# Performance work log

Measured on AMD Instinct MI355X. Metric: run time of the kernel, lower is better.

The kernel has to match this reference:

```python
import jax, jax.numpy as jnp
import numpy as np

N_HEAD = 16


def _rope_cos_sin(T, head_dim, dtype):
    inv_freq = 1.0 / (10000.0 ** (jnp.arange(0, head_dim, 2, dtype=jnp.float32) / head_dim))
    t = jnp.arange(T, dtype=jnp.float32)
    freqs = jnp.outer(t, inv_freq)  # [T, head_dim//2]
    return jnp.cos(freqs).astype(dtype), jnp.sin(freqs).astype(dtype)


def _apply_rope(x, cos, sin):
    # x: [B, H, T, D]; cos/sin: [T, D//2]
    x_even = x[..., ::2]
    x_odd = x[..., 1::2]
    c = cos[None, None, :, :]
    s = sin[None, None, :, :]
    out_even = x_even * c - x_odd * s
    out_odd = x_even * s + x_odd * c
    # interleave back: [..., D//2, 2] -> [..., D]
    return jnp.stack((out_even, out_odd), axis=-1).reshape(x.shape)


def setup_inputs() -> dict:
    key = jax.random.key(0)
    k1, k2, k3 = jax.random.split(key, 3)
    B, T, C = 2, 2048, 1024
    x = jax.random.normal(k1, (B, T, C), dtype=jnp.float32)
    w_qkv = jax.random.normal(k2, (C, 3 * C), dtype=jnp.float32) * (1.0 / np.sqrt(C))
    w_proj = jax.random.normal(k3, (C, C), dtype=jnp.float32) * (1.0 / np.sqrt(C))
    b_proj = jnp.zeros((C,), dtype=jnp.float32)
    return {"x": x, "w_qkv": w_qkv, "w_proj": w_proj, "b_proj": b_proj}


def reference(x, w_qkv, w_proj, b_proj):
    B, T, C = x.shape
    H = N_HEAD
    D = C // H
    qkv = x @ w_qkv  # [B, T, 3C]
    q, k, v = jnp.split(qkv, 3, axis=2)
    # [B, T, C] -> [B, H, T, D]
    q = q.reshape(B, T, H, D).transpose(0, 2, 1, 3)
    k = k.reshape(B, T, H, D).transpose(0, 2, 1, 3)
    v = v.reshape(B, T, H, D).transpose(0, 2, 1, 3)
    cos, sin = _rope_cos_sin(T, D, q.dtype)
    q = _apply_rope(q, cos, sin)
    k = _apply_rope(k, cos, sin)
    # causal SDPA
    scale = 1.0 / np.sqrt(D)
    att = jnp.einsum('bhqd,bhkd->bhqk', q, k) * scale
    causal = jnp.tril(jnp.ones((T, T), dtype=bool))
    att = jnp.where(causal[None, None, :, :], att, jnp.finfo(att.dtype).min)
    att = jax.nn.softmax(att, axis=-1)
    y = jnp.einsum('bhqk,bhkd->bhqd', att, v)  # [B, H, T, D]
    y = y.transpose(0, 2, 1, 3).reshape(B, T, C)
    return y @ w_proj + b_proj
```

## Files before the change

kernel.cpp:

```cpp
#include <hip/hip_runtime.h>
#include <math.h>

#define T_SEQ 2048
#define CDIM  1024
#define HEADS 16
#define DHEAD 64
#define BATCH 2
#define M_ROWS 4096
#define QSCALE 0.18033688011112042f

typedef unsigned short u16;
typedef unsigned int u32;
typedef __attribute__((ext_vector_type(8))) short bf16x8;
typedef __attribute__((ext_vector_type(4))) float f32x4;
typedef __attribute__((ext_vector_type(16))) float f32x16;

__device__ inline u16 f2bf(float f) {
    u32 u = __builtin_bit_cast(u32, f);
    u32 r = (u + 0x7fffu + ((u >> 16) & 1u)) >> 16;
    return (u16)r;
}

__device__ inline u32 cvtpk(float lo, float hi) {
    u32 r;
    asm("v_cvt_pk_bf16_f32 %0, %1, %2" : "=v"(r) : "v"(lo), "v"(hi));
    return r;
}

__device__ inline void permswap(u32& x, u32& y) {
    asm volatile("v_permlane32_swap_b32 %0, %1" : "+v"(x), "+v"(y));
}

__device__ inline float fexp2(float x) {
#if __has_builtin(__builtin_amdgcn_exp2f)
    return __builtin_amdgcn_exp2f(x);
#else
    float r; asm("v_exp_f32 %0, %1" : "=v"(r) : "v"(x)); return r;
#endif
}

__device__ inline void gload16(const void* g, void* l) {
    __builtin_amdgcn_global_load_lds(
        (const __attribute__((address_space(1))) void*)g,
        (__attribute__((address_space(3))) void*)l, 16, 0, 0);
}

__global__ void rope_table_kernel(float* __restrict__ cosT, float* __restrict__ sinT) {
    int idx = blockIdx.x * blockDim.x + threadIdx.x;
    if (idx >= T_SEQ * 32) return;
    int t = idx >> 5;
    int i = idx & 31;
    float expo = (2.0f * (float)i) / 64.0f;
    float inv = powf(10000.0f, -expo);
    float a = (float)t * inv;
    cosT[idx] = cosf(a);
    sinT[idx] = sinf(a);
}

__global__ __launch_bounds__(256)
void conv_bf16(const float* __restrict__ in, u16* __restrict__ out, int n8) {
    int i = blockIdx.x * blockDim.x + threadIdx.x;
    if (i >= n8) return;
    const float4* p = (const float4*)(in + (size_t)i * 8);
    float4 a = p[0], b = p[1];
    uint4 o;
    o.x = (u32)f2bf(a.x) | ((u32)f2bf(a.y) << 16);
    o.y = (u32)f2bf(a.z) | ((u32)f2bf(a.w) << 16);
    o.z = (u32)f2bf(b.x) | ((u32)f2bf(b.y) << 16);
    o.w = (u32)f2bf(b.z) | ((u32)f2bf(b.w) << 16);
    *(uint4*)(out + (size_t)i * 8) = o;
}

__global__ __launch_bounds__(256)
void convT64(const float* __restrict__ in, u16* __restrict__ out, int K, int N) {
    __shared__ float Ls[64][65];
    const int tid = threadIdx.x;
    const int k0 = blockIdx.y << 6, n0 = blockIdx.x << 6;
    const int r0 = tid >> 4, c4 = (tid & 15) << 2;
#pragma unroll
    for (int p = 0; p < 4; p++) {
        int r = r0 + (p << 4);
        float4 v = *(const float4*)&in[(size_t)(k0 + r) * N + n0 + c4];
        Ls[r][c4 + 0] = v.x; Ls[r][c4 + 1] = v.y;
        Ls[r][c4 + 2] = v.z; Ls[r][c4 + 3] = v.w;
    }
    __syncthreads();
    const int n = tid >> 2, kq = (tid & 3) << 4;
    u32 pk[8];
#pragma unroll
    for (int j = 0; j < 8; j++) {
        float lo = Ls[kq + 2 * j][n], hi = Ls[kq + 2 * j + 1][n];
        pk[j] = (u32)f2bf(lo) | ((u32)f2bf(hi) << 16);
    }
    u32* dst = (u32*)&out[(size_t)(n0 + n) * K + k0 + kq];
    ((uint4*)dst)[0] = make_uint4(pk[0], pk[1], pk[2], pk[3]);
    ((uint4*)dst)[1] = make_uint4(pk[4], pk[5], pk[6], pk[7]);
}

__global__ __launch_bounds__(256)
void transposeV(const u16* __restrict__ in, u16* __restrict__ out) {
    __shared__ u16 Ls[64][72];
    const int tid = threadIdx.x;
    const int bh = blockIdx.y;
    const int t0 = blockIdx.x << 6;
    const u16* src = in + ((size_t)bh << 17) + ((size_t)t0 << 6);
#pragma unroll
    for (int p = 0; p < 2; p++) {
        int L = tid + (p << 8);
        int t = L >> 3, c = L & 7;
        uint4 v = *(const uint4*)&src[(size_t)t * 64 + (c << 3)];
        *(uint4*)&Ls[t][c << 3] = v;
    }
    __syncthreads();
    const int d = tid >> 2, tq = (tid & 3) << 4;
    u32 pk[8];
#pragma unroll
    for (int j = 0; j < 8; j++) {
        u16 lo = Ls[tq + 2 * j][d], hi = Ls[tq + 2 * j + 1][d];
        pk[j] = (u32)lo | ((u32)hi << 16);
    }
    u16* dst = out + ((size_t)bh << 17) + ((size_t)d << 11) + t0 + tq;
    ((uint4*)dst)[0] = make_uint4(pk[0], pk[1], pk[2], pk[3]);
    ((uint4*)dst)[1] = make_uint4(pk[4], pk[5], pk[6], pk[7]);
}

template <int EPI>
__global__ __launch_bounds__(256)
void gemm_bf16(const u16* __restrict__ A, const u16* __restrict__ Bt,
               int N, int K,
               const float* __restrict__ bias, float* __restrict__ outF,
               u16* __restrict__ qOut, u16* __restrict__ kOut, u16* __restrict__ vOut,
               const float* __restrict__ cosT, const float* __restrict__ sinT) {
    __shared__ u16 Alds[2][128 * 32];
    __shared__ u16 Blds[2][128 * 32];
    const int tid = threadIdx.x;
    const int lane = tid & 63;
    const int w = tid >> 6;
    const int wr = w >> 1, wc = w & 1;
    const int g = lane >> 4, l15 = lane & 15;
    const int m0 = blockIdx.y * 128, n0 = blockIdx.x * 128;

    f32x4 acc[4][4];
#pragma unroll
    for (int m = 0; m < 4; m++)
#pragma unroll
        for (int n = 0; n < 4; n++)
#pragma unroll
            for (int e = 0; e < 4; e++) acc[m][n][e] = 0.f;

    int aoff[4], boff[4];
#pragma unroll
    for (int m = 0; m < 4; m++) {
        aoff[m] = ((wr << 6) + (m << 4) + l15) * 64 + (g << 4);
        boff[m] = ((wc << 6) + (m << 4) + l15) * 64 + (g << 4);
    }
    const int rowA0 = tid >> 2, kk0 = (tid & 3) << 3;

#define GSTAGE(BUF, K0)                                                          \
    {                                                                            \
        _Pragma("unroll") for (int pq = 0; pq < 2; pq++) {                       \
            int L = tid + (pq << 8);                                             \
            int row = rowA0 + (pq << 6);                                         \
            gload16(A + (size_t)(m0 + row) * K + (K0) + kk0, &Alds[BUF][0] + L * 8); \
            gload16(Bt + (size_t)(n0 + row) * K + (K0) + kk0, &Blds[BUF][0] + L * 8); \
        }                                                                        \
    }

    GSTAGE(0, 0);
    const int nt = K >> 5;
    int cur = 0;
    for (int t = 0; t < nt; t++) {
        if (t + 1 < nt) {
            GSTAGE(cur ^ 1, ((t + 1) << 5));
            asm volatile("s_waitcnt vmcnt(4)" ::: "memory");
        } else {
            asm volatile("s_waitcnt vmcnt(0)" ::: "memory");
        }
        __builtin_amdgcn_s_barrier();
        asm volatile("" ::: "memory");
        bf16x8 af[4], bfr[4];
#pragma unroll
        for (int m = 0; m < 4; m++) af[m] = *(const bf16x8*)((const char*)&Alds[cur][0] + aoff[m]);
#pragma unroll
        for (int n = 0; n < 4; n++) bfr[n] = *(const bf16x8*)((const char*)&Blds[cur][0] + boff[n]);
#pragma unroll
        for (int m = 0; m < 4; m++)
#pragma unroll
            for (int n = 0; n < 4; n++)
                acc[m][n] = __builtin_amdgcn_mfma_f32_16x16x32_bf16(af[m], bfr[n], acc[m][n], 0, 0, 0);
        asm volatile("" ::: "memory");
        __builtin_amdgcn_s_barrier();
        cur ^= 1;
    }
#undef GSTAGE

    if (EPI == 0) {
        const int sec = n0 >> 10;
#pragma unroll
        for (int m = 0; m < 4; m++) {
#pragma unroll
            for (int j = 0; j < 4; j++) {
                int t = m0 + (wr << 6) + (m << 4) + (g << 2) + j;
                int b = t >> 11, tt = t & 2047;
#pragma unroll
                for (int n = 0; n < 4; n++) {
                    int cc = (n0 + (wc << 6) + (n << 4) + l15) & 1023;
                    int h = cc >> 6, d = cc & 63;
                    float val = acc[m][n][j];
                    float o = val;
                    if (sec < 2) {
                        float partner = __shfl_xor(val, 1);
                        int i0 = d >> 1;
                        float c = cosT[tt * 32 + i0], s = sinT[tt * 32 + i0];
                        o = ((d & 1) == 0) ? (val * c - partner * s)
                                           : (partner * s + val * c);
                        if (sec == 0) o *= QSCALE;
                    }
                    size_t off = (((size_t)((b * 16 + h) * 2048 + tt)) << 6) + d;
                    u16* dst = (sec == 0) ? qOut : ((sec == 1) ? kOut : vOut);
                    dst[off] = f2bf(o);
                }
            }
        }
    } else {
#pragma unroll
        for (int m = 0; m < 4; m++) {
#pragma unroll
            for (int j = 0; j < 4; j++) {
                int t = m0 + (wr << 6) + (m << 4) + (g << 2) + j;
#pragma unroll
                for (int n = 0; n < 4; n++) {
                    int col = n0 + (wc << 6) + (n << 4) + l15;
                    outF[(size_t)t * N + col] = acc[m][n][j] + bias[col];
                }
            }
        }
    }
}

__device__ __forceinline__ void kv_stage2(const u16* Kb, const u16* Vtb,
                                          u16* Kl, u16* Vl, int tid, int k0) {
#pragma unroll
    for (int pp = 0; pp < 4; pp++) {
        int L = tid + (pp << 7);
        int row = L >> 3, c = L & 7;
        int cg = (c ^ (row & 7)) << 3;
        gload16(Kb + (((size_t)(k0 + row)) << 6) + cg, Kl + L * 8);
        gload16(Vtb + ((size_t)row << 11) + k0 + cg, Vl + L * 8);
    }
}

template <int NS>
__device__ __forceinline__ void attn_step32(
    const bf16x8 (&qf)[4], f32x16 (&O)[2], float& MR, float& LR,
    const char* Kl, const char* Vl, const int (&foff)[2][4],
    int lim, bool diag) {
    f32x16 st[NS];
#pragma unroll
    for (int s = 0; s < NS; s++) {
#pragma unroll
        for (int e = 0; e < 16; e++) st[s][e] = 0.f;
#pragma unroll
        for (int ks = 0; ks < 4; ks++) {
            bf16x8 kf = *(const bf16x8*)(Kl + foff[s][ks]);
            st[s] = __builtin_amdgcn_mfma_f32_32x32x16_bf16(kf, qf[ks], st[s], 0, 0, 0);
        }
    }
    if (diag) {
#pragma unroll
        for (int r = 0; r < 16; r++) {
            const int kvloc = (r & 3) + 8 * (r >> 2);
            if (kvloc > lim) st[NS - 1][r] = -1e30f;
        }
    }
    float t8[8];
#pragma unroll
    for (int r = 0; r < 8; r++) {
        float a = fmaxf(st[0][r], st[0][r + 8]);
        if (NS == 2) a = fmaxf(a, fmaxf(st[1][r], st[1][r + 8]));
        t8[r] = a;
    }
    float m = fmaxf(fmaxf(fmaxf(t8[0], t8[4]), fmaxf(t8[1], t8[5])),
                    fmaxf(fmaxf(t8[2], t8[6]), fmaxf(t8[3], t8[7])));
    m = fmaxf(m, __shfl_xor(m, 32));
    float mn = fmaxf(MR, m);
    if (__ballot(m - MR > 10.f)) {
        float al = fexp2(MR - mn);
        MR = mn;
        LR *= al;
#pragma unroll
        for (int e = 0; e < 16; e++) { O[0][e] *= al; O[1][e] *= al; }
    }
    float s0 = 0.f, s1 = 0.f, s2 = 0.f, s3 = 0.f;
#pragma unroll
    for (int s = 0; s < NS; s++)
#pragma unroll
        for (int r = 0; r < 16; r++) {
            float pv = fexp2(st[s][r] - MR);
            st[s][r] = pv;
            if ((r & 3) == 0) s0 += pv;
            else if ((r & 3) == 1) s1 += pv;
            else if ((r & 3) == 2) s2 += pv;
            else s3 += pv;
        }
    float sum = (s0 + s1) + (s2 + s3);
    sum += __shfl_xor(sum, 32);
    LR += sum;
#pragma unroll
    for (int ks = 0; ks < 2 * NS; ks++) {
        const int sT = ks >> 1, b1 = (ks & 1) << 3;
        u32 a = cvtpk(st[sT][b1 + 0], st[sT][b1 + 1]);
        u32 b = cvtpk(st[sT][b1 + 2], st[sT][b1 + 3]);
        u32 c = cvtpk(st[sT][b1 + 4], st[sT][b1 + 5]);
        u32 d = cvtpk(st[sT][b1 + 6], st[sT][b1 + 7]);
        permswap(a, c);
        permswap(b, d);
        bf16x8 pf = __builtin_bit_cast(bf16x8, make_uint4(a, b, c, d));
#pragma unroll
        for (int t2 = 0; t2 < 2; t2++) {
            bf16x8 vf = *(const bf16x8*)(Vl + foff[t2][ks]);
            O[t2] = __builtin_amdgcn_mfma_f32_32x32x16_bf16(vf, pf, O[t2], 0, 0, 0);
        }
    }
}

__device__ __forceinline__ void attn_store32(
    const f32x16 (&O)[2], float LR, u16* __restrict__ Yg,
    int b, int hd, int q, int hl) {
    float inv = 1.0f / LR;
    size_t rowoff = (((size_t)(b * 2048 + q)) << 10) + (hd << 6);
#pragma unroll
    for (int t2 = 0; t2 < 2; t2++)
#pragma unroll
        for (int rg = 0; rg < 4; rg++) {
            int d0 = (rg << 3) + (hl << 2) + (t2 << 5);
            u32 lo = cvtpk(O[t2][4 * rg + 0] * inv, O[t2][4 * rg + 1] * inv);
            u32 hi = cvtpk(O[t2][4 * rg + 2] * inv, O[t2][4 * rg + 3] * inv);
            *(uint2*)&Yg[rowoff + d0] = make_uint2(lo, hi);
        }
}

__global__ __launch_bounds__(128)
void attn_mfma(const u16* __restrict__ Qg, const u16* __restrict__ Kg,
               const u16* __restrict__ Vtg, u16* __restrict__ Yg) {
    __shared__ u16 Ks[2][64 * 64];
    __shared__ u16 Vts[2][64 * 64];

    const int tid = threadIdx.x;
    const int lane = tid & 63;
    const int w = tid >> 6;
    const int l31 = lane & 31, hl = lane >> 5;
    const int p = blockIdx.x;
    const int bh = blockIdx.y;
    const int b = bh >> 4, hd = bh & 15;
    const int qtA = p, qtB = 31 - p;
    const int lim = l31 - (hl << 2);

    const u16* Qb = Qg + ((size_t)bh << 17);
    const u16* Kb = Kg + ((size_t)bh << 17);
    const u16* Vtb = Vtg + ((size_t)bh << 17);

    int foff[2][4];
#pragma unroll
    for (int s = 0; s < 2; s++)
#pragma unroll
        for (int ks = 0; ks < 4; ks++) {
            int row = (s << 5) + l31;
            foff[s][ks] = row * 128 + (((hl + (ks << 1)) ^ (row & 7)) << 4);
        }

    const int qrA = (qtA << 6) + (w << 5) + l31;
    const int qrB = (qtB << 6) + (w << 5) + l31;
    bf16x8 qfA[4], qfB[4];
#pragma unroll
    for (int ks = 0; ks < 4; ks++) {
        int co = (hl << 3) + (ks << 4);
        qfA[ks] = *(const bf16x8*)(Qb + (((size_t)qrA) << 6) + co);
        qfB[ks] = *(const bf16x8*)(Qb + (((size_t)qrB) << 6) + co);
    }

    kv_stage2(Kb, Vtb, &Ks[0][0], &Vts[0][0], tid, 0);
    int cur = 0;

    f32x16 O[2];
    float MR, LR;

#pragma unroll
    for (int e = 0; e < 16; e++) { O[0][e] = 0.f; O[1][e] = 0.f; }
    MR = -1e30f; LR = 0.f;
    for (int kt = 0; kt <= qtA; kt++) {
        int nk0 = (kt < qtA) ? ((kt + 1) << 6) : 0;
        kv_stage2(Kb, Vtb, &Ks[cur ^ 1][0], &Vts[cur ^ 1][0], tid, nk0);
        asm volatile("s_waitcnt vmcnt(8)" ::: "memory");
        __builtin_amdgcn_s_barrier();
        asm volatile("" ::: "memory");
        if (kt == qtA) {
            if (w == 0)
                attn_step32<1>(qfA, O, MR, LR, (const char*)&Ks[cur][0],
                               (const char*)&Vts[cur][0], foff, lim, true);
            else
                attn_step32<2>(qfA, O, MR, LR, (const char*)&Ks[cur][0],
                               (const char*)&Vts[cur][0], foff, lim, true);
        } else {
            attn_step32<2>(qfA, O, MR, LR, (const char*)&Ks[cur][0],
                           (const char*)&Vts[cur][0], foff, lim, false);
        }
        asm volatile("" ::: "memory");
        __builtin_amdgcn_s_barrier();
        cur ^= 1;
    }
    attn_store32(O, LR, Yg, b, hd, qrA, hl);

#pragma unroll
    for (int e = 0; e < 16; e++) { O[0][e] = 0.f; O[1][e] = 0.f; }
    MR = -1e30f; LR = 0.f;
    for (int kt = 0; kt <= qtB; kt++) {
        if (kt < qtB) {
            kv_stage2(Kb, Vtb, &Ks[cur ^ 1][0], &Vts[cur ^ 1][0], tid, (kt + 1) << 6);
            asm volatile("s_waitcnt vmcnt(8)" ::: "memory");
        } else {
            asm volatile("s_waitcnt vmcnt(0)" ::: "memory");
        }
        __builtin_amdgcn_s_barrier();
        asm volatile("" ::: "memory");
        if (kt == qtB) {
            if (w == 0)
                attn_step32<1>(qfB, O, MR, LR, (const char*)&Ks[cur][0],
                               (const char*)&Vts[cur][0], foff, lim, true);
            else
                attn_step32<2>(qfB, O, MR, LR, (const char*)&Ks[cur][0],
                               (const char*)&Vts[cur][0], foff, lim, true);
        } else {
            attn_step32<2>(qfB, O, MR, LR, (const char*)&Ks[cur][0],
                           (const char*)&Vts[cur][0], foff, lim, false);
        }
        asm volatile("" ::: "memory");
        __builtin_amdgcn_s_barrier();
        cur ^= 1;
    }
    attn_store32(O, LR, Yg, b, hd, qrB, hl);
}

extern "C" void kernel_launch(void* const* d_in, const int* in_sizes, int n_in,
                              void* d_out, int out_size, void* d_ws, size_t ws_size,
                              hipStream_t stream) {
    const float* x      = (const float*)d_in[0];
    const float* w_qkv  = (const float*)d_in[1];
    const float* w_proj = (const float*)d_in[2];
    const float* b_proj = (const float*)d_in[3];
    float* out = (float*)d_out;

    const size_t SZ = (size_t)M_ROWS * CDIM;
    char* ws = (char*)d_ws;
    u16* xb     = (u16*)ws;                ws += SZ * 2;
    u16* wqkvT  = (u16*)ws;                ws += (size_t)3 * CDIM * CDIM * 2;
    u16* wprojT = (u16*)ws;                ws += (size_t)CDIM * CDIM * 2;
    u16* Qb     = (u16*)ws;                ws += SZ * 2;
    u16* Kb     = (u16*)ws;                ws += SZ * 2;
    u16* Vb     = (u16*)ws;                ws += SZ * 2;
    u16* Vt     = (u16*)ws;                ws += SZ * 2;
    u16* Yb     = (u16*)ws;                ws += SZ * 2;
    float* cosT = (float*)ws;              ws += (size_t)T_SEQ * 32 * 4;
    float* sinT = (float*)ws;              ws += (size_t)T_SEQ * 32 * 4;

    rope_table_kernel<<<dim3(256), dim3(256), 0, stream>>>(cosT, sinT);
    conv_bf16<<<dim3(2048), dim3(256), 0, stream>>>(x, xb, (int)(SZ / 8));
    convT64<<<dim3(48, 16), dim3(256), 0, stream>>>(w_qkv, wqkvT, CDIM, 3 * CDIM);
    convT64<<<dim3(16, 16), dim3(256), 0, stream>>>(w_proj, wprojT, CDIM, CDIM);

    gemm_bf16<0><<<dim3(24, 32), dim3(256), 0, stream>>>(
        xb, wqkvT, 3 * CDIM, CDIM, nullptr, nullptr, Qb, Kb, Vb, cosT, sinT);

    transposeV<<<dim3(32, 32), dim3(256), 0, stream>>>(Vb, Vt);

    attn_mfma<<<dim3(16, 32), dim3(128), 0, stream>>>(Qb, Kb, Vt, Yb);

    gemm_bf16<1><<<dim3(8, 32), dim3(256), 0, stream>>>(
        Yb, wprojT, CDIM, CDIM, b_proj, out, nullptr, nullptr, nullptr, nullptr, nullptr);
}
```

Measured before the change: 230.2 us.

## Restructure causal attention into 128-row query blocks with 4 waves per block

Replaces the paired-tile attention scheme (2 waves, each block walking a short and a long query tile) with one 128-query block of 4 waves that share each staged K/V tile. Blocks are launched longest-first by reversing the query-block index, and waves skip or mask tiles according to their own 32-row slice. s_setprio hints are added around the MFMA sections. The aim is to halve K/V staging traffic per query and raise occupancy. The cost is more blocks with uneven work and some wave idling on diagonal tiles.

```diff
diff --git a/kernel.cpp b/kernel.cpp
--- a/kernel.cpp
+++ b/kernel.cpp
@@ -241,8 +241,8 @@
 __device__ __forceinline__ void kv_stage2(const u16* Kb, const u16* Vtb,
                                           u16* Kl, u16* Vl, int tid, int k0) {
 #pragma unroll
-    for (int pp = 0; pp < 4; pp++) {
-        int L = tid + (pp << 7);
+    for (int pp = 0; pp < 2; pp++) {
+        int L = tid + (pp << 8);
         int row = L >> 3, c = L & 7;
         int cg = (c ^ (row & 7)) << 3;
         gload16(Kb + (((size_t)(k0 + row)) << 6) + cg, Kl + L * 8);
@@ -250,14 +250,14 @@
     }
 }
 
-template <int NS>
+template <bool MASKED>
 __device__ __forceinline__ void attn_step32(
     const bf16x8 (&qf)[4], f32x16 (&O)[2], float& MR, float& LR,
-    const char* Kl, const char* Vl, const int (&foff)[2][4],
-    int lim, bool diag) {
-    f32x16 st[NS];
-#pragma unroll
-    for (int s = 0; s < NS; s++) {
+    const char* Kl, const char* Vl, const int (&foff)[2][4], int lim) {
+    f32x16 st[2];
+    __builtin_amdgcn_s_setprio(1);
+#pragma unroll
+    for (int s = 0; s < 2; s++) {
 #pragma unroll
         for (int e = 0; e < 16; e++) st[s][e] = 0.f;
 #pragma unroll
@@ -266,20 +266,23 @@
             st[s] = __builtin_amdgcn_mfma_f32_32x32x16_bf16(kf, qf[ks], st[s], 0, 0, 0);
         }
     }
-    if (diag) {
-#pragma unroll
-        for (int r = 0; r < 16; r++) {
-            const int kvloc = (r & 3) + 8 * (r >> 2);
-            if (kvloc > lim) st[NS - 1][r] = -1e30f;
+    __builtin_amdgcn_s_setprio(0);
+    if (MASKED) {
+#pragma unroll
+        for (int s = 0; s < 2; s++) {
+            const int ls = lim - (s << 5);
+#pragma unroll
+            for (int r = 0; r < 16; r++) {
+                const int kvloc = (r & 3) + 8 * (r >> 2);
+                if (kvloc > ls) st[s][r] = -1e30f;
+            }
         }
     }
     float t8[8];
 #pragma unroll
-    for (int r = 0; r < 8; r++) {
-        float a = fmaxf(st[0][r], st[0][r + 8]);
-        if (NS == 2) a = fmaxf(a, fmaxf(st[1][r], st[1][r + 8]));
-        t8[r] = a;
-    }
+    for (int r = 0; r < 8; r++)
+        t8[r] = fmaxf(fmaxf(st[0][r], st[0][r + 8]),
+                      fmaxf(st[1][r], st[1][r + 8]));
     float m = fmaxf(fmaxf(fmaxf(t8[0], t8[4]), fmaxf(t8[1], t8[5])),
                     fmaxf(fmaxf(t8[2], t8[6]), fmaxf(t8[3], t8[7])));
     m = fmaxf(m, __shfl_xor(m, 32));
@@ -293,7 +296,7 @@
     }
     float s0 = 0.f, s1 = 0.f, s2 = 0.f, s3 = 0.f;
 #pragma unroll
-    for (int s = 0; s < NS; s++)
+    for (int s = 0; s < 2; s++)
 #pragma unroll
         for (int r = 0; r < 16; r++) {
             float pv = fexp2(st[s][r] - MR);
@@ -307,7 +310,7 @@
     sum += __shfl_xor(sum, 32);
     LR += sum;
 #pragma unroll
-    for (int ks = 0; ks < 2 * NS; ks++) {
+    for (int ks = 0; ks < 4; ks++) {
         const int sT = ks >> 1, b1 = (ks & 1) << 3;
         u32 a = cvtpk(st[sT][b1 + 0], st[sT][b1 + 1]);
         u32 b = cvtpk(st[sT][b1 + 2], st[sT][b1 + 3]);
@@ -316,11 +319,13 @@
         permswap(a, c);
         permswap(b, d);
         bf16x8 pf = __builtin_bit_cast(bf16x8, make_uint4(a, b, c, d));
+        __builtin_amdgcn_s_setprio(1);
 #pragma unroll
         for (int t2 = 0; t2 < 2; t2++) {
             bf16x8 vf = *(const bf16x8*)(Vl + foff[t2][ks]);
             O[t2] = __builtin_amdgcn_mfma_f32_32x32x16_bf16(vf, pf, O[t2], 0, 0, 0);
         }
+        __builtin_amdgcn_s_setprio(0);
     }
 }
 
@@ -340,7 +345,7 @@
         }
 }
 
-__global__ __launch_bounds__(128)
+__global__ __launch_bounds__(256)
 void attn_mfma(const u16* __restrict__ Qg, const u16* __restrict__ Kg,
                const u16* __restrict__ Vtg, u16* __restrict__ Yg) {
     __shared__ u16 Ks[2][64 * 64];
@@ -350,11 +355,12 @@
     const int lane = tid & 63;
     const int w = tid >> 6;
     const int l31 = lane & 31, hl = lane >> 5;
-    const int p = blockIdx.x;
-    const int bh = blockIdx.y;
+    const int bh = (int)blockIdx.x;
+    const int Qi = (int)gridDim.y - 1 - (int)blockIdx.y;
     const int b = bh >> 4, hd = bh & 15;
-    const int qtA = p, qtB = 31 - p;
-    const int lim = l31 - (hl << 2);
+    const int qbw = (Qi << 7) + (w << 5);
+    const int q_lane = qbw + l31;
+    const int nst = 2 * Qi + 2;
 
     const u16* Qb = Qg + ((size_t)bh << 17);
     const u16* Kb = Kg + ((size_t)bh << 17);
@@ -369,76 +375,44 @@
             foff[s][ks] = row * 128 + (((hl + (ks << 1)) ^ (row & 7)) << 4);
         }
 
-    const int qrA = (qtA << 6) + (w << 5) + l31;
-    const int qrB = (qtB << 6) + (w << 5) + l31;
-    bf16x8 qfA[4], qfB[4];
-#pragma unroll
-    for (int ks = 0; ks < 4; ks++) {
-        int co = (hl << 3) + (ks << 4);
-        qfA[ks] = *(const bf16x8*)(Qb + (((size_t)qrA) << 6) + co);
-        qfB[ks] = *(const bf16x8*)(Qb + (((size_t)qrB) << 6) + co);
-    }
+    bf16x8 qf[4];
+#pragma unroll
+    for (int ks = 0; ks < 4; ks++)
+        qf[ks] = *(const bf16x8*)(Qb + (((size_t)q_lane) << 6) + (hl << 3) + (ks << 4));
+
+    f32x16 O[2];
+#pragma unroll
+    for (int e = 0; e < 16; e++) { O[0][e] = 0.f; O[1][e] = 0.f; }
+    float MR = -1e30f, LR = 0.f;
 
     kv_stage2(Kb, Vtb, &Ks[0][0], &Vts[0][0], tid, 0);
     int cur = 0;
 
-    f32x16 O[2];
-    float MR, LR;
-
-#pragma unroll
-    for (int e = 0; e < 16; e++) { O[0][e] = 0.f; O[1][e] = 0.f; }
-    MR = -1e30f; LR = 0.f;
-    for (int kt = 0; kt <= qtA; kt++) {
-        int nk0 = (kt < qtA) ? ((kt + 1) << 6) : 0;
-        kv_stage2(Kb, Vtb, &Ks[cur ^ 1][0], &Vts[cur ^ 1][0], tid, nk0);
-        asm volatile("s_waitcnt vmcnt(8)" ::: "memory");
+    for (int kt = 0; kt < nst; kt++) {
+        if (kt + 1 < nst) {
+            kv_stage2(Kb, Vtb, &Ks[cur ^ 1][0], &Vts[cur ^ 1][0], tid, (kt + 1) << 6);
+            asm volatile("s_waitcnt vmcnt(4)" ::: "memory");
+        } else {
+            asm volatile("s_waitcnt vmcnt(0)" ::: "memory");
+        }
         __builtin_amdgcn_s_barrier();
         asm volatile("" ::: "memory");
-        if (kt == qtA) {
-            if (w == 0)
-                attn_step32<1>(qfA, O, MR, LR, (const char*)&Ks[cur][0],
-                               (const char*)&Vts[cur][0], foff, lim, true);
-            else
-                attn_step32<2>(qfA, O, MR, LR, (const char*)&Ks[cur][0],
-                               (const char*)&Vts[cur][0], foff, lim, true);
-        } else {
-            attn_step32<2>(qfA, O, MR, LR, (const char*)&Ks[cur][0],
-                           (const char*)&Vts[cur][0], foff, lim, false);
+        const int kv0 = kt << 6;
+        if (kv0 <= qbw + 31) {
+            if (qbw - kv0 >= 63) {
+                attn_step32<false>(qf, O, MR, LR, (const char*)&Ks[cur][0],
+                                   (const char*)&Vts[cur][0], foff, 0);
+            } else {
+                int lim = q_lane - kv0 - (hl << 2);
+                attn_step32<true>(qf, O, MR, LR, (const char*)&Ks[cur][0],
+                                  (const char*)&Vts[cur][0], foff, lim);
+            }
         }
         asm volatile("" ::: "memory");
         __builtin_amdgcn_s_barrier();
         cur ^= 1;
     }
-    attn_store32(O, LR, Yg, b, hd, qrA, hl);
-
-#pragma unroll
-    for (int e = 0; e < 16; e++) { O[0][e] = 0.f; O[1][e] = 0.f; }
-    MR = -1e30f; LR = 0.f;
-    for (int kt = 0; kt <= qtB; kt++) {
-        if (kt < qtB) {
-            kv_stage2(Kb, Vtb, &Ks[cur ^ 1][0], &Vts[cur ^ 1][0], tid, (kt + 1) << 6);
-            asm volatile("s_waitcnt vmcnt(8)" ::: "memory");
-        } else {
-            asm volatile("s_waitcnt vmcnt(0)" ::: "memory");
-        }
-        __builtin_amdgcn_s_barrier();
-        asm volatile("" ::: "memory");
-        if (kt == qtB) {
-            if (w == 0)
-                attn_step32<1>(qfB, O, MR, LR, (const char*)&Ks[cur][0],
-                               (const char*)&Vts[cur][0], foff, lim, true);
-            else
-                attn_step32<2>(qfB, O, MR, LR, (const char*)&Ks[cur][0],
-                               (const char*)&Vts[cur][0], foff, lim, true);
-        } else {
-            attn_step32<2>(qfB, O, MR, LR, (const char*)&Ks[cur][0],
-                           (const char*)&Vts[cur][0], foff, lim, false);
-        }
-        asm volatile("" ::: "memory");
-        __builtin_amdgcn_s_barrier();
-        cur ^= 1;
-    }
-    attn_store32(O, LR, Yg, b, hd, qrB, hl);
+    attn_store32(O, LR, Yg, b, hd, q_lane, hl);
 }
 
 extern "C" void kernel_launch(void* const* d_in, const int* in_sizes, int n_in,
@@ -473,7 +447,7 @@
 
     transposeV<<<dim3(32, 32), dim3(256), 0, stream>>>(Vb, Vt);
 
-    attn_mfma<<<dim3(16, 32), dim3(128), 0, stream>>>(Qb, Kb, Vt, Yb);
+    attn_mfma<<<dim3(32, 16), dim3(256), 0, stream>>>(Qb, Kb, Vt, Yb);
 
     gemm_bf16<1><<<dim3(8, 32), dim3(256), 0, stream>>>(
         Yb, wprojT, CDIM, CDIM, b_proj, out, nullptr, nullptr, nullptr, nullptr, nullptr);
```

After: 213.2 us. 7.4% less time.
